# Performance work log

Measured on AMD Instinct MI355X. Metric: run time of the kernel, lower is better.

## Reference

```python
import jax, jax.numpy as jnp
import numpy as np
from jax import lax

# db6 orthogonal wavelet: reconstruction low-pass filter (pywt rec_lo), L=12 taps
_H = np.array([
    0.11154074335008017, 0.4946238903983854, 0.7511339080215775,
    0.3152503517092432, -0.22626469396516913, -0.12976686756709563,
    0.09750160558707936, 0.02752286553001629, -0.031582039318031156,
    0.0005538422009938016, 0.004777257511010651, -0.00107730108499558])
_L = 12
_RLO = _H
_RHI = _H[::-1].copy(); _RHI[1::2] *= -1.0  # pywt qmf -> rec_hi
# pytorch_wavelets afb1d cross-correlates with time-reversed dec filters == rec filters
_ANA = np.stack([_RLO, _RHI])                       # [2, L] analysis (stride-2 corr)
_SYN = np.stack([_RLO[::-1], _RHI[::-1]])           # [2, L] synthesis (transposed conv as corr with flipped rec)
_LEVEL = 4


def _afb1d(x, axis):
    """Single-level analysis along `axis` with symmetric padding (pytorch_wavelets semantics)."""
    x = jnp.moveaxis(x, axis, -1)
    N = x.shape[-1]
    out = (N + _L - 1) // 2                  # pywt.dwt_coeff_len, symmetric mode
    p = 2 * (out - 1) - N + _L
    pad = [(0, 0)] * (x.ndim - 1) + [(p // 2, (p + 1) // 2)]
    xp = jnp.pad(x, pad, mode='symmetric')
    lead = xp.shape[:-1]
    xf = xp.reshape(-1, 1, xp.shape[-1])
    k = jnp.asarray(_ANA, x.dtype)[:, None, :]          # [2,1,L]
    y = lax.conv_general_dilated(xf, k, (2,), 'VALID',
                                 dimension_numbers=('NCH', 'OIH', 'NCH'))  # [Bf,2,out]
    y = y.reshape(*lead, 2, out)
    lo = jnp.moveaxis(y[..., 0, :], -1, axis)
    hi = jnp.moveaxis(y[..., 1, :], -1, axis)
    return lo, hi


def _sfb1d(lo, hi, axis):
    """Single-level synthesis along `axis`: stride-2 transposed conv, crop L-2 each side."""
    lo = jnp.moveaxis(lo, axis, -1)
    hi = jnp.moveaxis(hi, axis, -1)
    lead = lo.shape[:-1]
    N = lo.shape[-1]
    xf = jnp.stack([lo.reshape(-1, N), hi.reshape(-1, N)], axis=1)  # [Bf,2,N]
    k = jnp.asarray(_SYN, lo.dtype)[None, :, :]                     # [1,2,L]
    y = lax.conv_general_dilated(xf, k, (1,), [(1, 1)], lhs_dilation=(2,),
                                 dimension_numbers=('NCH', 'OIH', 'NCH'))  # [Bf,1,2N+2-L]
    y = y[:, 0].reshape(*lead, 2 * N + 2 - _L)
    return jnp.moveaxis(y, -1, axis)


def _dwt2(x, J):
    ll, yh = x, []
    for _ in range(J):
        lo, hi = _afb1d(ll, -1)          # filter rows (W)
        ll, lh = _afb1d(lo, -2)          # filter cols (H): band order LL, LH, HL, HH
        hl, hh = _afb1d(hi, -2)
        yh.append(jnp.stack([lh, hl, hh], axis=2))  # [B,C,3,h,w]
    return ll, yh


def _idwt2(yl, yh):
    ll = yl
    for h in yh[::-1]:
        if ll.shape[-2] > h.shape[-2]:
            ll = ll[..., :-1, :]
        if ll.shape[-1] > h.shape[-1]:
            ll = ll[..., :-1]
        lo = _sfb1d(ll, h[:, :, 0], -2)
        hi = _sfb1d(h[:, :, 1], h[:, :, 2], -2)
        ll = _sfb1d(lo, hi, -1)
    return ll


def setup_inputs() -> dict:
    key = jax.random.key(0)
    k0, k1, k2 = jax.random.split(key, 3)
    B, CIN, COUT, HW = 8, 32, 32, 512
    HC = 42  # coarse size after 4 db6 symmetric levels: 512->261->136->73->42
    scale = 1.0 / (CIN * COUT)
    x = jax.random.normal(k0, (B, CIN, HW, HW), dtype=jnp.float32)
    w_yl = scale * jax.random.uniform(k1, (CIN, COUT, HC, HC), dtype=jnp.float32)
    w_yh = scale * jax.random.uniform(k2, (CIN, COUT, 3, HC, HC), dtype=jnp.float32)
    return {"x": x, "w_yl": w_yl, "w_yh": w_yh}


def reference(x, w_yl, w_yh):
    yl, yh = _dwt2(x, _LEVEL)
    yl_out = jnp.einsum('bixy,ioxy->boxy', yl, w_yl)
    yh_out = yh[:-1] + [jnp.einsum('bicxy,iocxy->bocxy', yh[-1], w_yh)]
    return _idwt2(yl_out, yh_out)
```

## Files before the change

kernel.cpp:

```cpp
#include <hip/hip_runtime.h>

#define FL 12

__constant__ float c_ana_lo[FL] = {
    0.11154074335008017f,  0.4946238903983854f,   0.7511339080215775f,   0.3152503517092432f,
   -0.22626469396516913f, -0.12976686756709563f,  0.09750160558707936f,  0.02752286553001629f,
   -0.031582039318031156f, 0.0005538422009938016f, 0.004777257511010651f, -0.00107730108499558f };
__constant__ float c_ana_hi[FL] = {
   -0.00107730108499558f, -0.004777257511010651f, 0.0005538422009938016f, 0.031582039318031156f,
    0.02752286553001629f, -0.09750160558707936f, -0.12976686756709563f,   0.22626469396516913f,
    0.3152503517092432f,  -0.7511339080215775f,   0.4946238903983854f,   -0.11154074335008017f };
__constant__ float c_syn_lo[FL] = {
   -0.00107730108499558f,  0.004777257511010651f, 0.0005538422009938016f, -0.031582039318031156f,
    0.02752286553001629f,  0.09750160558707936f, -0.12976686756709563f,  -0.22626469396516913f,
    0.3152503517092432f,   0.7511339080215775f,   0.4946238903983854f,    0.11154074335008017f };
__constant__ float c_syn_hi[FL] = {
   -0.11154074335008017f,  0.4946238903983854f,  -0.7511339080215775f,    0.3152503517092432f,
    0.22626469396516913f, -0.12976686756709563f, -0.09750160558707936f,   0.02752286553001629f,
    0.031582039318031156f, 0.0005538422009938016f, -0.004777257511010651f, -0.00107730108499558f };

__device__ __forceinline__ int symi(int i, int N) {
    i = (i < 0) ? (-1 - i) : i;
    i = (i >= N) ? (2 * N - 1 - i) : i;
    return i;
}

template<bool BOTH>
__global__ __launch_bounds__(256) void afb_row(const float* __restrict__ in, float* __restrict__ lo,
                                               float* __restrict__ hi, int N, int Nout) {
    __shared__ float row[512];
    const int r = blockIdx.x;
    const float* src = in + (size_t)r * N;
    if ((N & 3) == 0) {
        const float4* s4 = (const float4*)src;
        float4* r4 = (float4*)row;
        for (int j = threadIdx.x; j < (N >> 2); j += 256) r4[j] = s4[j];
    } else {
        for (int j = threadIdx.x; j < N; j += 256) row[j] = src[j];
    }
    __syncthreads();
    const int padL = (2 * (Nout - 1) - N + FL) >> 1;
    for (int t = threadIdx.x; t < Nout; t += 256) {
        int j0 = 2 * t - padL;
        float alo = 0.f, ahi = 0.f;
        if (j0 >= 0 && j0 + FL <= N) {
            const float* w = &row[j0];
#pragma unroll
            for (int k = 0; k < FL; k++) {
                float v = w[k];
                alo += v * c_ana_lo[k];
                if (BOTH) ahi += v * c_ana_hi[k];
            }
        } else {
#pragma unroll
            for (int k = 0; k < FL; k++) {
                float v = row[symi(j0 + k, N)];
                alo += v * c_ana_lo[k];
                if (BOTH) ahi += v * c_ana_hi[k];
            }
        }
        lo[(size_t)r * Nout + t] = alo;
        if (BOTH) hi[(size_t)r * Nout + t] = ahi;
    }
}

template<bool BOTH>
__global__ __launch_bounds__(256) void afb_col(const float* __restrict__ in, float* __restrict__ lo,
                                               float* __restrict__ hi, int Hin, int Hout, int W, int total) {
    int idx = blockIdx.x * 256 + threadIdx.x;
    if (idx >= total) return;
    int x = idx % W;
    int rw = idx / W;
    int t = rw % Hout;
    int img = rw / Hout;
    const float* src = in + (size_t)img * Hin * W + x;
    const int padL = (2 * (Hout - 1) - Hin + FL) >> 1;
    int j0 = 2 * t - padL;
    float alo = 0.f, ahi = 0.f;
    if (j0 >= 0 && j0 + FL <= Hin) {
        const float* p = src + (size_t)j0 * W;
#pragma unroll
        for (int k = 0; k < FL; k++) {
            float v = p[(size_t)k * W];
            alo += v * c_ana_lo[k];
            if (BOTH) ahi += v * c_ana_hi[k];
        }
    } else {
#pragma unroll
        for (int k = 0; k < FL; k++) {
            float v = src[(size_t)symi(j0 + k, Hin) * W];
            alo += v * c_ana_lo[k];
            if (BOTH) ahi += v * c_ana_hi[k];
        }
    }
    lo[idx] = alo;
    if (BOTH) hi[idx] = ahi;
}

template<bool TWO>
__global__ __launch_bounds__(256) void sfb_col(const float* __restrict__ lo, const float* __restrict__ hi,
                                               float* __restrict__ out, int rowStride, int imgStride,
                                               int W, int Hout, int total) {
    int idx = blockIdx.x * 256 + threadIdx.x;
    if (idx >= total) return;
    int x = idx % W;
    int rw = idx / W;
    int t = rw % Hout;
    int img = rw / Hout;
    const float* plo = lo + (size_t)img * imgStride + x;
    const float* phi = TWO ? hi + (size_t)img * imgStride + x : plo;
    int m0 = t >> 1;
    int odd = t & 1;
    float wl[6], wh[6];
#pragma unroll
    for (int d = 0; d < 6; d++) {
        wl[d] = odd ? c_syn_lo[2 * d] : c_syn_lo[2 * d + 1];
        if (TWO) wh[d] = odd ? c_syn_hi[2 * d] : c_syn_hi[2 * d + 1];
    }
    float acc = 0.f;
#pragma unroll
    for (int d = 0; d < 6; d++) {
        int m = m0 + d;
        float a = plo[(size_t)m * rowStride] * wl[d];
        if (TWO) a += phi[(size_t)m * rowStride] * wh[d];
        acc += a;
    }
    out[idx] = acc;
}

template<bool TWO>
__global__ __launch_bounds__(256) void sfb_row(const float* __restrict__ lo, const float* __restrict__ hi,
                                               float* __restrict__ out, int Nin, int Wout) {
    __shared__ float slo[136];
    __shared__ float shi[136];
    const int r = blockIdx.x;
    const float* pl = lo + (size_t)r * Nin;
    const float* ph = TWO ? hi + (size_t)r * Nin : pl;
    for (int j = threadIdx.x; j < Nin; j += 256) {
        slo[j] = pl[j];
        if (TWO) shi[j] = ph[j];
    }
    __syncthreads();
    for (int t = threadIdx.x; t < Wout; t += 256) {
        int m0 = t >> 1;
        int odd = t & 1;
        float wl[6], wh[6];
#pragma unroll
        for (int d = 0; d < 6; d++) {
            wl[d] = odd ? c_syn_lo[2 * d] : c_syn_lo[2 * d + 1];
            if (TWO) wh[d] = odd ? c_syn_hi[2 * d] : c_syn_hi[2 * d + 1];
        }
        float acc = 0.f;
#pragma unroll
        for (int d = 0; d < 6; d++) {
            acc += slo[m0 + d] * wl[d];
            if (TWO) acc += shi[m0 + d] * wh[d];
        }
        out[(size_t)r * Wout + t] = acc;
    }
}

__global__ __launch_bounds__(256) void mix_bands(float* __restrict__ yl, float* __restrict__ lh,
                                                 float* __restrict__ hl, float* __restrict__ hh,
                                                 const float* __restrict__ w_yl, const float* __restrict__ w_yh) {
    const int P = 1764;
    int blk = blockIdx.x;
    int tile = blk % 221;
    int b = (blk / 221) % 8;
    int c = blk / (221 * 8);
    float* band = (c == 0) ? yl : (c == 1) ? lh : (c == 2) ? hl : hh;
    int p0 = tile * 8;
    __shared__ float sb[256];
    int i = threadIdx.x >> 3;
    int dp = threadIdx.x & 7;
    int p = p0 + dp;
    sb[threadIdx.x] = (p < P) ? band[(size_t)(b * 32 + i) * P + p] : 0.f;
    __syncthreads();
    int o = i;
    if (p < P) {
        float acc = 0.f;
        if (c == 0) {
#pragma unroll 4
            for (int ii = 0; ii < 32; ii++)
                acc += sb[(ii << 3) | dp] * w_yl[(size_t)(ii * 32 + o) * P + p];
        } else {
            const float* wb = w_yh + (size_t)(c - 1) * P;
#pragma unroll 4
            for (int ii = 0; ii < 32; ii++)
                acc += sb[(ii << 3) | dp] * wb[(size_t)(ii * 32 + o) * 3 * P + p];
        }
        acc -= sb[(o << 3) | dp];
        band[(size_t)(b * 32 + o) * P + p] = acc;
    }
}

__global__ __launch_bounds__(256) void final_fuse(const float* __restrict__ u2, const float* __restrict__ x,
                                                  float* __restrict__ out) {
    __shared__ float t1row[261];
    int img = blockIdx.x >> 9;
    int y = blockIdx.x & 511;
    const float* pu = u2 + (size_t)img * 262 * 262;
    int m0y = y >> 1;
    int oddy = y & 1;
    float wy[6];
#pragma unroll
    for (int d = 0; d < 6; d++)
        wy[d] = oddy ? c_syn_lo[2 * d] : c_syn_lo[2 * d + 1];
    for (int xc = threadIdx.x; xc < 261; xc += 256) {
        float acc = 0.f;
#pragma unroll
        for (int d = 0; d < 6; d++)
            acc += pu[(size_t)(m0y + d) * 262 + xc] * wy[d];
        t1row[xc] = acc;
    }
    __syncthreads();
    const float* px = x + ((size_t)img * 512 + y) * 512;
    float* po = out + ((size_t)img * 512 + y) * 512;
    for (int t = threadIdx.x; t < 512; t += 256) {
        int m0 = t >> 1;
        int odd = t & 1;
        float wl[6];
#pragma unroll
        for (int d = 0; d < 6; d++)
            wl[d] = odd ? c_syn_lo[2 * d] : c_syn_lo[2 * d + 1];
        float acc = px[t];
#pragma unroll
        for (int d = 0; d < 6; d++)
            acc += t1row[m0 + d] * wl[d];
        po[t] = acc;
    }
}

extern "C" void kernel_launch(void* const* d_in, const int* in_sizes, int n_in,
                              void* d_out, int out_size, void* d_ws, size_t ws_size,
                              hipStream_t stream) {
    (void)in_sizes; (void)n_in; (void)out_size; (void)ws_size;
    const float* x = (const float*)d_in[0];
    const float* w_yl = (const float*)d_in[1];
    const float* w_yh = (const float*)d_in[2];
    float* out = (float*)d_out;
    float* ws = (float*)d_ws;

    float* loW1 = out;
    float* ll1 = out + 34209792;

    float* u2  = ws;
    float* slC = ws + 17572864;
    float* slD = slC + 9121792;
    float* slE = slD + 4734976;
    float* slF = slE + 2541568;
    float* g1  = slF + 1401856;
    float* g2  = g1 + 795648;
    float* g3  = g2 + 795648;
    float* g4  = g3 + 451584;
    float* g5  = g4 + 451584;
    float* g6  = g5 + 451584;

    dim3 B(256);
    afb_row<false><<<256 * 512, B, 0, stream>>>(x, loW1, nullptr, 512, 261);
    { int tot = 256 * 261 * 261; afb_col<false><<<(tot + 255) / 256, B, 0, stream>>>(loW1, ll1, nullptr, 512, 261, 261, tot); }
    afb_row<false><<<256 * 261, B, 0, stream>>>(ll1, slC, nullptr, 261, 136);
    { int tot = 256 * 136 * 136; afb_col<false><<<(tot + 255) / 256, B, 0, stream>>>(slC, slD, nullptr, 261, 136, 136, tot); }
    afb_row<false><<<256 * 136, B, 0, stream>>>(slD, slE, nullptr, 136, 73);
    { int tot = 256 * 73 * 73; afb_col<false><<<(tot + 255) / 256, B, 0, stream>>>(slE, slF, nullptr, 136, 73, 73, tot); }
    afb_row<true><<<256 * 73, B, 0, stream>>>(slF, g1, g2, 73, 42);
    { int tot = 256 * 42 * 42; afb_col<true><<<(tot + 255) / 256, B, 0, stream>>>(g1, g3, g4, 73, 42, 42, tot); }
    { int tot = 256 * 42 * 42; afb_col<true><<<(tot + 255) / 256, B, 0, stream>>>(g2, g5, g6, 73, 42, 42, tot); }

    mix_bands<<<4 * 8 * 221, B, 0, stream>>>(g3, g4, g5, g6, w_yl, w_yh);

    { int tot = 256 * 74 * 42; sfb_col<true><<<(tot + 255) / 256, B, 0, stream>>>(g3, g4, g1, 42, 42 * 42, 42, 74, tot); }
    { int tot = 256 * 74 * 42; sfb_col<true><<<(tot + 255) / 256, B, 0, stream>>>(g5, g6, g2, 42, 42 * 42, 42, 74, tot); }
    sfb_row<true><<<256 * 74, B, 0, stream>>>(g1, g2, slF, 42, 74);
    { int tot = 256 * 136 * 73; sfb_col<false><<<(tot + 255) / 256, B, 0, stream>>>(slF, nullptr, slE, 74, 74 * 74, 73, 136, tot); }
    sfb_row<false><<<256 * 136, B, 0, stream>>>(slE, nullptr, slD, 73, 136);
    { int tot = 256 * 262 * 136; sfb_col<false><<<(tot + 255) / 256, B, 0, stream>>>(slD, nullptr, slC, 136, 136 * 136, 136, 262, tot); }
    sfb_row<false><<<256 * 262, B, 0, stream>>>(slC, nullptr, u2, 136, 262);

    final_fuse<<<256 * 512, B, 0, stream>>>(u2, x, out);
}
```

Before: 1.140 ms.

## Fuse last row synthesis into final kernel with 8-row tiles in shared memory

Drops the separate sfb_row launch that wrote the 262x262 u2 intermediate. The final kernel now computes the needed u2 rows directly from slC into shared memory. Each block handles 8 output rows instead of one, so the intermediate rows are reused across the vertical synthesis. This removes a full write and read of u2 and one launch, at the cost of more shared memory, extra registers for the prefetched x values, and some recomputation of u2 rows at tile borders.

```diff
diff --git a/kernel.cpp b/kernel.cpp
--- a/kernel.cpp
+++ b/kernel.cpp
@@ -194,40 +194,70 @@
     }
 }
 
-__global__ __launch_bounds__(256) void final_fuse(const float* __restrict__ u2, const float* __restrict__ x,
+__global__ __launch_bounds__(256) void final_fuse(const float* __restrict__ slC, const float* __restrict__ x,
                                                   float* __restrict__ out) {
-    __shared__ float t1row[261];
-    int img = blockIdx.x >> 9;
-    int y = blockIdx.x & 511;
-    const float* pu = u2 + (size_t)img * 262 * 262;
-    int m0y = y >> 1;
-    int oddy = y & 1;
-    float wy[6];
-#pragma unroll
-    for (int d = 0; d < 6; d++)
-        wy[d] = oddy ? c_syn_lo[2 * d] : c_syn_lo[2 * d + 1];
-    for (int xc = threadIdx.x; xc < 261; xc += 256) {
+    __shared__ float u2t[9][262];
+    __shared__ float t1[8][262];
+    int img = blockIdx.x >> 6;
+    int q = blockIdx.x & 63;
+    int y0 = q << 3;
+    int mBase = q << 2;
+    const float* pc = slC + (size_t)img * 262 * 136;
+    const float* px = x + ((size_t)img * 512 + y0) * 512;
+    float* po = out + ((size_t)img * 512 + y0) * 512;
+
+    float xv[16];
+#pragma unroll
+    for (int yy = 0; yy < 8; yy++) {
+        xv[2 * yy]     = px[(size_t)yy * 512 + threadIdx.x];
+        xv[2 * yy + 1] = px[(size_t)yy * 512 + threadIdx.x + 256];
+    }
+
+    for (int e = threadIdx.x; e < 9 * 262; e += 256) {
+        int mp = e / 262;
+        int xc = e - mp * 262;
+        const float* pr = pc + (size_t)(mBase + mp) * 136 + (xc >> 1);
+        int odd = xc & 1;
         float acc = 0.f;
 #pragma unroll
-        for (int d = 0; d < 6; d++)
-            acc += pu[(size_t)(m0y + d) * 262 + xc] * wy[d];
-        t1row[xc] = acc;
-    }
-    __syncthreads();
-    const float* px = x + ((size_t)img * 512 + y) * 512;
-    float* po = out + ((size_t)img * 512 + y) * 512;
-    for (int t = threadIdx.x; t < 512; t += 256) {
-        int m0 = t >> 1;
-        int odd = t & 1;
-        float wl[6];
-#pragma unroll
-        for (int d = 0; d < 6; d++)
-            wl[d] = odd ? c_syn_lo[2 * d] : c_syn_lo[2 * d + 1];
-        float acc = px[t];
-#pragma unroll
-        for (int d = 0; d < 6; d++)
-            acc += t1row[m0 + d] * wl[d];
-        po[t] = acc;
+        for (int d = 0; d < 6; d++) {
+            float w = odd ? c_syn_lo[2 * d] : c_syn_lo[2 * d + 1];
+            acc += pr[d] * w;
+        }
+        u2t[0][e] = acc;
+    }
+    __syncthreads();
+
+    for (int e = threadIdx.x; e < 8 * 262; e += 256) {
+        int yy = e / 262;
+        int xc = e - yy * 262;
+        int m0 = yy >> 1;
+        int odd = yy & 1;
+        float acc = 0.f;
+#pragma unroll
+        for (int d = 0; d < 6; d++) {
+            float w = odd ? c_syn_lo[2 * d] : c_syn_lo[2 * d + 1];
+            acc += u2t[m0 + d][xc] * w;
+        }
+        t1[0][e] = acc;
+    }
+    __syncthreads();
+
+    int odd = threadIdx.x & 1;
+    float wl[6];
+#pragma unroll
+    for (int d = 0; d < 6; d++) wl[d] = odd ? c_syn_lo[2 * d] : c_syn_lo[2 * d + 1];
+#pragma unroll
+    for (int yy = 0; yy < 8; yy++) {
+#pragma unroll
+        for (int h = 0; h < 2; h++) {
+            int t = threadIdx.x + (h << 8);
+            int m0 = t >> 1;
+            float acc = xv[2 * yy + h];
+#pragma unroll
+            for (int d = 0; d < 6; d++) acc += t1[yy][m0 + d] * wl[d];
+            po[(size_t)yy * 512 + t] = acc;
+        }
     }
 }
 
@@ -244,7 +274,6 @@
     float* loW1 = out;
     float* ll1 = out + 34209792;
 
-    float* u2  = ws;
     float* slC = ws + 17572864;
     float* slD = slC + 9121792;
     float* slE = slD + 4734976;
@@ -275,7 +304,6 @@
     { int tot = 256 * 136 * 73; sfb_col<false><<<(tot + 255) / 256, B, 0, stream>>>(slF, nullptr, slE, 74, 74 * 74, 73, 136, tot); }
     sfb_row<false><<<256 * 136, B, 0, stream>>>(slE, nullptr, slD, 73, 136);
     { int tot = 256 * 262 * 136; sfb_col<false><<<(tot + 255) / 256, B, 0, stream>>>(slD, nullptr, slC, 136, 136 * 136, 136, 262, tot); }
-    sfb_row<false><<<256 * 262, B, 0, stream>>>(slC, nullptr, u2, 136, 262);
-
-    final_fuse<<<256 * 512, B, 0, stream>>>(u2, x, out);
-}
+
+    final_fuse<<<256 * 64, B, 0, stream>>>(slC, x, out);
+}
```

Result: faster. 1.020 ms (-10.5%).
